# Kernel tuning notes

Hardware: AMD Instinct MI355X
Metric: run time of the kernel (lower is better)

Reference implementation:

```python
import jax, jax.numpy as jnp
import numpy as np

B, L, D, H = 2, 2048, 1024, 16
DK = D // H  # 64


def setup_inputs() -> dict:
    key = jax.random.key(0)
    ks = jax.random.split(key, 9)
    s = 0.02
    return {
        "x": jax.random.normal(ks[0], (B, L, D), dtype=jnp.float32),
        "wq": jax.random.normal(ks[1], (D, D), dtype=jnp.float32) * s,
        "bq": jax.random.normal(ks[2], (D,), dtype=jnp.float32) * s,
        "wk": jax.random.normal(ks[3], (D, D), dtype=jnp.float32) * s,
        "bk": jax.random.normal(ks[4], (D,), dtype=jnp.float32) * s,
        "wv": jax.random.normal(ks[5], (D, D), dtype=jnp.float32) * s,
        "bv": jax.random.normal(ks[6], (D,), dtype=jnp.float32) * s,
        "wo": jax.random.normal(ks[7], (D, D), dtype=jnp.float32) * s,
        "bo": jax.random.normal(ks[8], (D,), dtype=jnp.float32) * s,
    }


def reference(x, wq, bq, wk, bk, wv, bv, wo, bo):
    b, l, d = x.shape
    # torch nn.Linear: y = x @ W^T + b
    q = (x @ wq.T + bq).reshape(b, l, H, DK).transpose(0, 2, 1, 3)  # (b,h,l,dk)
    k = (x @ wk.T + bk).reshape(b, l, H, DK).transpose(0, 2, 1, 3)
    v = (x @ wv.T + bv).reshape(b, l, H, DK).transpose(0, 2, 1, 3)
    scale = 1.0 / jnp.sqrt(jnp.asarray(DK, dtype=x.dtype))
    scores = jnp.einsum("bhqd,bhkd->bhqk", q, k) * scale  # (b,h,l,l)
    causal = jnp.triu(jnp.ones((l, l), dtype=bool), k=1)  # True above diagonal -> masked
    scores = jnp.where(causal[None, None], -jnp.inf, scores)
    probs = jax.nn.softmax(scores, axis=-1)
    out = jnp.einsum("bhqk,bhkd->bhqd", probs, v)  # (b,h,l,dk)
    out = out.transpose(0, 2, 1, 3).reshape(b, l, d)
    return out @ wo.T + bo
```

## Files before the change

### kernel.cpp

```cpp
#include <hip/hip_runtime.h>
#include <cstdint>

#define SEQ     2048
#define DMODEL  1024
#define NHEAD   16
#define DKH     64
#define NTOK    4096
#define LDQKV   3072

typedef __bf16 bf16x8 __attribute__((ext_vector_type(8)));
typedef __bf16 bf16x4 __attribute__((ext_vector_type(4)));
typedef float  f32x4  __attribute__((ext_vector_type(4)));

#define MFMA_BF16(a, b, c) __builtin_amdgcn_mfma_f32_16x16x32_bf16((a), (b), (c), 0, 0, 0)

#define C2F 0.18033688f

__device__ inline float fast_exp2(float x) {
#if __has_builtin(__builtin_amdgcn_exp2f)
  return __builtin_amdgcn_exp2f(x);
#else
  return __expf(x * 0.69314718056f);
#endif
}

__device__ inline void async_copy16(const void* g, void* l) {
  __builtin_amdgcn_global_load_lds(
      reinterpret_cast<const __attribute__((address_space(1))) void*>(
          reinterpret_cast<uintptr_t>(g)),
      reinterpret_cast<__attribute__((address_space(3))) void*>(
          reinterpret_cast<uintptr_t>(l)),
      16, 0, 0);
}

__device__ inline bf16x4 cvt4(float4 v) {
  bf16x4 r;
  r[0] = (__bf16)v.x; r[1] = (__bf16)v.y; r[2] = (__bf16)v.z; r[3] = (__bf16)v.w;
  return r;
}

__global__ __launch_bounds__(256) void pack_kernel(
    const float4* __restrict__ x,
    const float4* __restrict__ wq, const float4* __restrict__ wk,
    const float4* __restrict__ wv, const float4* __restrict__ wo,
    const float4* __restrict__ bq, const float4* __restrict__ bk,
    const float4* __restrict__ bv,
    bf16x4* __restrict__ xb, bf16x4* __restrict__ wqkv,
    bf16x4* __restrict__ wob, float4* __restrict__ bcat)
{
  const int NX = NTOK * DMODEL / 4;
  const int NW = DMODEL * DMODEL / 4;
  const int TOT = NX + 4 * NW + 3 * (DMODEL / 4);
  for (int g = blockIdx.x * 256 + threadIdx.x; g < TOT; g += gridDim.x * 256) {
    if (g < NX) {
      xb[g] = cvt4(x[g]);
    } else if (g < NX + 3 * NW) {
      int g2 = g - NX;
      const float4* s = (g2 < NW) ? wq : (g2 < 2 * NW ? wk : wv);
      float4 v = s[g2 & (NW - 1)];
      if (g2 < NW) { v.x *= C2F; v.y *= C2F; v.z *= C2F; v.w *= C2F; }
      wqkv[g2] = cvt4(v);
    } else if (g < NX + 4 * NW) {
      int g3 = g - NX - 3 * NW;
      wob[g3] = cvt4(wo[g3]);
    } else {
      int g4 = g - NX - 4 * NW;
      const float4* s = (g4 < 256) ? bq : (g4 < 512 ? bk : bv);
      float4 v = s[g4 & 255];
      if (g4 < 256) { v.x *= C2F; v.y *= C2F; v.z *= C2F; v.w *= C2F; }
      bcat[g4] = v;
    }
  }
}

template<int BN>
__global__ __launch_bounds__(256) void gemm_bias(
    const __bf16* __restrict__ A, const __bf16* __restrict__ W,
    const float* __restrict__ bias, void* __restrict__ C,
    int ldc, int out_bf16)
{
  constexpr int K = 1024;
  constexpr int JT = BN / 32;
  __shared__ __bf16 sA[2][128 * 32];
  __shared__ __bf16 sB[2][BN * 32];
  const int tid  = threadIdx.x;
  const int wave = tid >> 6, lane = tid & 63;
  const int quad = lane >> 4, l16 = lane & 15;
  const size_t m0 = (size_t)blockIdx.x * 128;
  const size_t n0 = (size_t)blockIdx.y * BN;
  const int wm = (wave & 1) * 64, wn = (wave >> 1) * (BN / 2);

  const int g0 = wave * 2;
  const int sr = lane >> 2;
  const int sc = (lane & 3) * 8;
  const __bf16* pa0 = A + (m0 + g0 * 16 + sr) * K + sc;
  const __bf16* pa1 = pa0 + 16 * K;
  const int brow = (BN == 128) ? g0 * 16 : wave * 16;
  const __bf16* pb0 = W + (n0 + brow + sr) * K + sc;
  const int lo  = g0 * 512;
  const int lob = (BN == 128) ? g0 * 512 : wave * 512;

  f32x4 acc[4][JT];
  const f32x4 z = {0.f, 0.f, 0.f, 0.f};
#pragma unroll
  for (int i = 0; i < 4; ++i)
#pragma unroll
    for (int j = 0; j < JT; ++j) acc[i][j] = z;

  async_copy16(pa0, &sA[0][lo]);
  async_copy16(pa1, &sA[0][lo + 512]);
  async_copy16(pb0, &sB[0][lob]);
  if (BN == 128) async_copy16(pb0 + 16 * K, &sB[0][lob + 512]);

  for (int k0 = 0; k0 < K; k0 += 32) {
    const int cur = (k0 >> 5) & 1, nxt = cur ^ 1;
    __syncthreads();
    if (k0 + 32 < K) {
      async_copy16(pa0 + k0 + 32, &sA[nxt][lo]);
      async_copy16(pa1 + k0 + 32, &sA[nxt][lo + 512]);
      async_copy16(pb0 + k0 + 32, &sB[nxt][lob]);
      if (BN == 128) async_copy16(pb0 + 16 * K + k0 + 32, &sB[nxt][lob + 512]);
    }

    bf16x8 af[4], bw[JT];
#pragma unroll
    for (int i = 0; i < 4; ++i)
      af[i] = *(const bf16x8*)(&sA[cur][(wm + i * 16 + l16) * 32 + quad * 8]);
#pragma unroll
    for (int j = 0; j < JT; ++j)
      bw[j] = *(const bf16x8*)(&sB[cur][(wn + j * 16 + l16) * 32 + quad * 8]);
#pragma unroll
    for (int i = 0; i < 4; ++i)
#pragma unroll
      for (int j = 0; j < JT; ++j)
        acc[i][j] = MFMA_BF16(af[i], bw[j], acc[i][j]);
  }

  float bi[JT];
#pragma unroll
  for (int j = 0; j < JT; ++j) bi[j] = bias[n0 + wn + j * 16 + l16];

#pragma unroll
  for (int i = 0; i < 4; ++i) {
#pragma unroll
    for (int j = 0; j < JT; ++j) {
#pragma unroll
      for (int r = 0; r < 4; ++r) {
        size_t row = m0 + wm + i * 16 + quad * 4 + r;
        size_t col = n0 + wn + j * 16 + l16;
        float v = acc[i][j][r] + bi[j];
        if (out_bf16) ((__bf16*)C)[row * ldc + col] = (__bf16)v;
        else          ((float*)C)[row * ldc + col] = v;
      }
    }
  }
}

__global__ __launch_bounds__(256) void vtrans_kernel(
    const __bf16* __restrict__ qkv, __bf16* __restrict__ vt)
{
  __shared__ __bf16 t[64][66];
  const int tid = threadIdx.x;
  const int bh = blockIdx.x;
  const int b = bh >> 4, h = bh & 15;
  const int l0 = blockIdx.y * 64;
  const int r4 = tid >> 6;
  const int c  = tid & 63;
#pragma unroll
  for (int rep = 0; rep < 16; ++rep) {
    int ll = rep * 4 + r4;
    t[ll][c] = qkv[(size_t)(b * SEQ + l0 + ll) * LDQKV + 2048 + h * DKH + c];
  }
  __syncthreads();
#pragma unroll
  for (int rep = 0; rep < 16; ++rep) {
    int dk = rep * 4 + r4;
    vt[(size_t)(bh * DKH + dk) * SEQ + l0 + c] = t[c][dk];
  }
}

__global__ __launch_bounds__(256) void attn_kernel(
    const __bf16* __restrict__ qkv,
    const __bf16* __restrict__ vt,
    __bf16* __restrict__ attn)
{
  __shared__ __bf16 sK[2][64 * 64];
  __shared__ __bf16 sV[2][64 * 64];
  __shared__ __bf16 pbuf[4][16 * 64];
  const int tid  = threadIdx.x;
  const int wave = tid >> 6, lane = tid & 63;
  const int quad = lane >> 4, l16 = lane & 15;
  const int id = blockIdx.x;
  const int u = (id >> 3) & 31, v = id & 7, w = id >> 8;
  const int bh = v * 4 + w;
  const int ue = u ^ ((w >> 1) << 3);
  const int qb = (w & 1) ? ue : 31 - ue;
  const int b = bh >> 4, h = bh & 15;
  const int q0 = qb * 64;
  const int qw = q0 + wave * 16;
  const size_t tokbase = (size_t)b * SEQ;

  const int srow = lane >> 3;
  const int sgr  = (lane & 7) ^ srow;
  const __bf16* pKsrc = qkv + (tokbase + wave * 16 + srow) * LDQKV + 1024 + h * DKH + sgr * 8;
  const __bf16* pVsrc = vt + ((size_t)bh * DKH + wave * 16 + srow) * SEQ + sgr * 8;
  const int lo = wave * 16 * 64;

  bf16x8 qf[2];
#pragma unroll
  for (int s = 0; s < 2; ++s)
    qf[s] = *(const bf16x8*)(qkv + (tokbase + qw + l16) * LDQKV + h * DKH + s * 32 + quad * 8);

  bf16x8 ones;
#pragma unroll
  for (int i = 0; i < 8; ++i) ones[i] = (__bf16)1.0f;

  f32x4 o[4], lacc;
  const f32x4 z = {0.f, 0.f, 0.f, 0.f};
#pragma unroll
  for (int t = 0; t < 4; ++t) o[t] = z;
  lacc = z;

  __bf16* pb = &pbuf[wave][0];
  const int swl = l16 & 7;

  async_copy16(pKsrc, &sK[0][lo]);
  async_copy16(pKsrc + (size_t)8 * LDQKV, &sK[0][lo + 8 * 64]);
  async_copy16(pVsrc, &sV[0][lo]);
  async_copy16(pVsrc + (size_t)8 * SEQ, &sV[0][lo + 8 * 64]);

  for (int t0 = 0; t0 <= qb; ++t0) {
    const int cur = t0 & 1, nxt = cur ^ 1;
    __syncthreads();
    if (t0 < qb) {
      const size_t koff = (size_t)(t0 + 1) * 64;
      async_copy16(pKsrc + koff * LDQKV, &sK[nxt][lo]);
      async_copy16(pKsrc + (koff + 8) * LDQKV, &sK[nxt][lo + 8 * 64]);
      async_copy16(pVsrc + koff, &sV[nxt][lo]);
      async_copy16(pVsrc + (size_t)8 * SEQ + koff, &sV[nxt][lo + 8 * 64]);
    }
    const __bf16* K_ = &sK[cur][0];
    const __bf16* V_ = &sV[cur][0];

    f32x4 sacc[4];
#pragma unroll
    for (int ct = 0; ct < 4; ++ct) {
      bf16x8 k0 = *(const bf16x8*)(K_ + (ct * 16 + l16) * 64 + ((quad ^ swl) * 8));
      bf16x8 k1 = *(const bf16x8*)(K_ + (ct * 16 + l16) * 64 + (((4 + quad) ^ swl) * 8));
      sacc[ct] = MFMA_BF16(k0, qf[0], z);
      sacc[ct] = MFMA_BF16(k1, qf[1], sacc[ct]);
    }

#pragma unroll
    for (int ct = 0; ct < 4; ++ct) {
      bf16x4 p4;
      if (t0 < qb) {
#pragma unroll
        for (int r = 0; r < 4; ++r) p4[r] = (__bf16)fast_exp2(sacc[ct][r]);
      } else {
#pragma unroll
        for (int r = 0; r < 4; ++r) {
          float sv = (ct * 16 + quad * 4 + r <= wave * 16 + l16) ? sacc[ct][r] : -1e30f;
          p4[r] = (__bf16)fast_exp2(sv);
        }
      }
      *(bf16x4*)(pb + l16 * 64 + (((ct * 4 + quad) ^ (swl << 1)) * 4)) = p4;
    }
    bf16x8 ap0 = *(const bf16x8*)(pb + l16 * 64 + ((quad ^ swl) * 8));
    bf16x8 ap1 = *(const bf16x8*)(pb + l16 * 64 + (((4 + quad) ^ swl) * 8));

    lacc = MFMA_BF16(ap0, ones, lacc);
    lacc = MFMA_BF16(ap1, ones, lacc);

#pragma unroll
    for (int dt = 0; dt < 4; ++dt) {
      bf16x8 v0 = *(const bf16x8*)(V_ + (dt * 16 + l16) * 64 + ((quad ^ swl) * 8));
      bf16x8 v1 = *(const bf16x8*)(V_ + (dt * 16 + l16) * 64 + (((4 + quad) ^ swl) * 8));
      o[dt] = MFMA_BF16(ap0, v0, o[dt]);
      o[dt] = MFMA_BF16(ap1, v1, o[dt]);
    }
  }

  float linv[4];
#pragma unroll
  for (int r = 0; r < 4; ++r) linv[r] = 1.0f / lacc[r];

#pragma unroll
  for (int dt = 0; dt < 4; ++dt)
#pragma unroll
    for (int r = 0; r < 4; ++r)
      attn[(tokbase + qw + quad * 4 + r) * DMODEL + h * DKH + dt * 16 + l16] =
          (__bf16)(o[dt][r] * linv[r]);
}

extern "C" void kernel_launch(void* const* d_in, const int* in_sizes, int n_in,
                              void* d_out, int out_size, void* d_ws, size_t ws_size,
                              hipStream_t stream) {
  const float* x  = (const float*)d_in[0];
  const float* wq = (const float*)d_in[1];
  const float* bq = (const float*)d_in[2];
  const float* wk = (const float*)d_in[3];
  const float* bk = (const float*)d_in[4];
  const float* wv = (const float*)d_in[5];
  const float* bv = (const float*)d_in[6];
  const float* wo = (const float*)d_in[7];
  const float* bo = (const float*)d_in[8];

  char* ws = (char*)d_ws;
  __bf16* xb    = (__bf16*)(ws + 0);
  __bf16* wqkv  = (__bf16*)(ws + 8388608);
  __bf16* wob   = (__bf16*)(ws + 14680064);
  float*  bcat  = (float*)(ws + 16777216);
  __bf16* qkv   = (__bf16*)(ws + 16789504);
  __bf16* vt    = (__bf16*)(ws + 41955328);
  __bf16* attn  = (__bf16*)(ws + 50343936);
  float*  out   = (float*)d_out;

  pack_kernel<<<1024, 256, 0, stream>>>(
      (const float4*)x, (const float4*)wq, (const float4*)wk, (const float4*)wv,
      (const float4*)wo, (const float4*)bq, (const float4*)bk, (const float4*)bv,
      (bf16x4*)xb, (bf16x4*)wqkv, (bf16x4*)wob, (float4*)bcat);

  gemm_bias<128><<<dim3(32, 24), 256, 0, stream>>>(xb, wqkv, bcat, qkv, LDQKV, 1);

  vtrans_kernel<<<dim3(32, 32), 256, 0, stream>>>(qkv, vt);

  attn_kernel<<<1024, 256, 0, stream>>>(qkv, vt, attn);

  gemm_bias<64><<<dim3(32, 16), 256, 0, stream>>>(attn, wob, bo, out, DMODEL, 0);
}
```

Baseline: 177.4 us.

## Enlarge attention query tile to 128 rows, two 16-row halves per wave

Each attention block now handles 128 query rows instead of 64, with every wave owning two 16-row halves, and the grid is halved to 512 blocks. Each K/V tile loaded into shared memory and each K/V fragment read from LDS now feeds twice as many MFMAs, cutting K/V traffic and per-tile sync overhead per query. The cost is more registers per thread (two sets of accumulators and Q fragments), a doubled P buffer, fewer blocks for load balancing, and wasted masked work on diagonal tiles.

```diff
diff --git a/kernel.cpp b/kernel.cpp
--- a/kernel.cpp
+++ b/kernel.cpp
@@ -186,18 +186,18 @@
 {
   __shared__ __bf16 sK[2][64 * 64];
   __shared__ __bf16 sV[2][64 * 64];
-  __shared__ __bf16 pbuf[4][16 * 64];
+  __shared__ __bf16 pbuf[4][2][16 * 64];
   const int tid  = threadIdx.x;
   const int wave = tid >> 6, lane = tid & 63;
   const int quad = lane >> 4, l16 = lane & 15;
   const int id = blockIdx.x;
-  const int u = (id >> 3) & 31, v = id & 7, w = id >> 8;
+  const int u = (id >> 3) & 15, v = id & 7, w = id >> 7;
   const int bh = v * 4 + w;
-  const int ue = u ^ ((w >> 1) << 3);
-  const int qb = (w & 1) ? ue : 31 - ue;
+  const int ue = u ^ ((w >> 1) * 15);
+  const int qb = (w & 1) ? ue : 15 - ue;
   const int b = bh >> 4, h = bh & 15;
-  const int q0 = qb * 64;
-  const int qw = q0 + wave * 16;
+  const int q0 = qb * 128;
+  const int qw = q0 + wave * 32;
   const size_t tokbase = (size_t)b * SEQ;
 
   const int srow = lane >> 3;
@@ -206,33 +206,40 @@
   const __bf16* pVsrc = vt + ((size_t)bh * DKH + wave * 16 + srow) * SEQ + sgr * 8;
   const int lo = wave * 16 * 64;
 
-  bf16x8 qf[2];
-#pragma unroll
-  for (int s = 0; s < 2; ++s)
-    qf[s] = *(const bf16x8*)(qkv + (tokbase + qw + l16) * LDQKV + h * DKH + s * 32 + quad * 8);
+  bf16x8 qf[2][2];
+#pragma unroll
+  for (int hf = 0; hf < 2; ++hf)
+#pragma unroll
+    for (int s = 0; s < 2; ++s)
+      qf[hf][s] = *(const bf16x8*)(qkv + (tokbase + qw + hf * 16 + l16) * LDQKV
+                                   + h * DKH + s * 32 + quad * 8);
 
   bf16x8 ones;
 #pragma unroll
   for (int i = 0; i < 8; ++i) ones[i] = (__bf16)1.0f;
 
-  f32x4 o[4], lacc;
+  f32x4 o[2][4], lacc[2];
   const f32x4 z = {0.f, 0.f, 0.f, 0.f};
 #pragma unroll
-  for (int t = 0; t < 4; ++t) o[t] = z;
-  lacc = z;
-
-  __bf16* pb = &pbuf[wave][0];
+  for (int hf = 0; hf < 2; ++hf) {
+#pragma unroll
+    for (int t = 0; t < 4; ++t) o[hf][t] = z;
+    lacc[hf] = z;
+  }
+
   const int swl = l16 & 7;
+  const int ntiles = 2 * qb + 2;
 
   async_copy16(pKsrc, &sK[0][lo]);
   async_copy16(pKsrc + (size_t)8 * LDQKV, &sK[0][lo + 8 * 64]);
   async_copy16(pVsrc, &sV[0][lo]);
   async_copy16(pVsrc + (size_t)8 * SEQ, &sV[0][lo + 8 * 64]);
 
-  for (int t0 = 0; t0 <= qb; ++t0) {
+  for (int t0 = 0; t0 < ntiles; ++t0) {
     const int cur = t0 & 1, nxt = cur ^ 1;
+    const int key0 = t0 * 64;
     __syncthreads();
-    if (t0 < qb) {
+    if (t0 + 1 < ntiles) {
       const size_t koff = (size_t)(t0 + 1) * 64;
       async_copy16(pKsrc + koff * LDQKV, &sK[nxt][lo]);
       async_copy16(pKsrc + (koff + 8) * LDQKV, &sK[nxt][lo + 8 * 64]);
@@ -242,55 +249,73 @@
     const __bf16* K_ = &sK[cur][0];
     const __bf16* V_ = &sV[cur][0];
 
-    f32x4 sacc[4];
+    f32x4 sacc[2][4];
 #pragma unroll
     for (int ct = 0; ct < 4; ++ct) {
       bf16x8 k0 = *(const bf16x8*)(K_ + (ct * 16 + l16) * 64 + ((quad ^ swl) * 8));
       bf16x8 k1 = *(const bf16x8*)(K_ + (ct * 16 + l16) * 64 + (((4 + quad) ^ swl) * 8));
-      sacc[ct] = MFMA_BF16(k0, qf[0], z);
-      sacc[ct] = MFMA_BF16(k1, qf[1], sacc[ct]);
-    }
-
-#pragma unroll
-    for (int ct = 0; ct < 4; ++ct) {
-      bf16x4 p4;
-      if (t0 < qb) {
-#pragma unroll
-        for (int r = 0; r < 4; ++r) p4[r] = (__bf16)fast_exp2(sacc[ct][r]);
-      } else {
-#pragma unroll
-        for (int r = 0; r < 4; ++r) {
-          float sv = (ct * 16 + quad * 4 + r <= wave * 16 + l16) ? sacc[ct][r] : -1e30f;
-          p4[r] = (__bf16)fast_exp2(sv);
+#pragma unroll
+      for (int hf = 0; hf < 2; ++hf) {
+        sacc[hf][ct] = MFMA_BF16(k0, qf[hf][0], z);
+        sacc[hf][ct] = MFMA_BF16(k1, qf[hf][1], sacc[hf][ct]);
+      }
+    }
+
+    const bool fullv = (key0 + 63 <= qw);
+#pragma unroll
+    for (int hf = 0; hf < 2; ++hf) {
+      __bf16* pb = &pbuf[wave][hf][0];
+#pragma unroll
+      for (int ct = 0; ct < 4; ++ct) {
+        bf16x4 p4;
+        if (fullv) {
+#pragma unroll
+          for (int r = 0; r < 4; ++r) p4[r] = (__bf16)fast_exp2(sacc[hf][ct][r]);
+        } else {
+#pragma unroll
+          for (int r = 0; r < 4; ++r) {
+            float sv = (key0 + ct * 16 + quad * 4 + r <= qw + hf * 16 + l16)
+                           ? sacc[hf][ct][r] : -1e30f;
+            p4[r] = (__bf16)fast_exp2(sv);
+          }
         }
+        *(bf16x4*)(pb + l16 * 64 + (((ct * 4 + quad) ^ (swl << 1)) * 4)) = p4;
       }
-      *(bf16x4*)(pb + l16 * 64 + (((ct * 4 + quad) ^ (swl << 1)) * 4)) = p4;
-    }
-    bf16x8 ap0 = *(const bf16x8*)(pb + l16 * 64 + ((quad ^ swl) * 8));
-    bf16x8 ap1 = *(const bf16x8*)(pb + l16 * 64 + (((4 + quad) ^ swl) * 8));
-
-    lacc = MFMA_BF16(ap0, ones, lacc);
-    lacc = MFMA_BF16(ap1, ones, lacc);
-
+    }
+
+    bf16x8 ap[2][2];
+#pragma unroll
+    for (int hf = 0; hf < 2; ++hf) {
+      const __bf16* pb = &pbuf[wave][hf][0];
+      ap[hf][0] = *(const bf16x8*)(pb + l16 * 64 + ((quad ^ swl) * 8));
+      ap[hf][1] = *(const bf16x8*)(pb + l16 * 64 + (((4 + quad) ^ swl) * 8));
+      lacc[hf] = MFMA_BF16(ap[hf][0], ones, lacc[hf]);
+      lacc[hf] = MFMA_BF16(ap[hf][1], ones, lacc[hf]);
+    }
 #pragma unroll
     for (int dt = 0; dt < 4; ++dt) {
       bf16x8 v0 = *(const bf16x8*)(V_ + (dt * 16 + l16) * 64 + ((quad ^ swl) * 8));
       bf16x8 v1 = *(const bf16x8*)(V_ + (dt * 16 + l16) * 64 + (((4 + quad) ^ swl) * 8));
-      o[dt] = MFMA_BF16(ap0, v0, o[dt]);
-      o[dt] = MFMA_BF16(ap1, v1, o[dt]);
-    }
-  }
-
-  float linv[4];
-#pragma unroll
-  for (int r = 0; r < 4; ++r) linv[r] = 1.0f / lacc[r];
-
-#pragma unroll
-  for (int dt = 0; dt < 4; ++dt)
-#pragma unroll
-    for (int r = 0; r < 4; ++r)
-      attn[(tokbase + qw + quad * 4 + r) * DMODEL + h * DKH + dt * 16 + l16] =
-          (__bf16)(o[dt][r] * linv[r]);
+#pragma unroll
+      for (int hf = 0; hf < 2; ++hf) {
+        o[hf][dt] = MFMA_BF16(ap[hf][0], v0, o[hf][dt]);
+        o[hf][dt] = MFMA_BF16(ap[hf][1], v1, o[hf][dt]);
+      }
+    }
+  }
+
+#pragma unroll
+  for (int hf = 0; hf < 2; ++hf) {
+    float linv[4];
+#pragma unroll
+    for (int r = 0; r < 4; ++r) linv[r] = 1.0f / lacc[hf][r];
+#pragma unroll
+    for (int dt = 0; dt < 4; ++dt)
+#pragma unroll
+      for (int r = 0; r < 4; ++r)
+        attn[(tokbase + qw + hf * 16 + quad * 4 + r) * DMODEL + h * DKH + dt * 16 + l16] =
+            (__bf16)(o[hf][dt][r] * linv[r]);
+  }
 }
 
 extern "C" void kernel_launch(void* const* d_in, const int* in_sizes, int n_in,
@@ -325,7 +350,7 @@
 
   vtrans_kernel<<<dim3(32, 32), 256, 0, stream>>>(qkv, vt);
 
-  attn_kernel<<<1024, 256, 0, stream>>>(qkv, vt, attn);
+  attn_kernel<<<512, 256, 0, stream>>>(qkv, vt, attn);
 
   gemm_bias<64><<<dim3(32, 16), 256, 0, stream>>>(attn, wob, bo, out, DMODEL, 0);
 }
```

New measurement: 185.5 us. 1.05x slower.
